# Performance work log

Hardware: AMD Instinct MI355X
Metric: run time of the kernel (lower is better)

## Reference

```python
import jax, jax.numpy as jnp
import numpy as np

NUM_NODES = 10000
WINDOW = 8
IN_C = 8
HID = 64
N_TOT = WINDOW * NUM_NODES
N_EDGES = 1280000
EPS = 1e-5


def setup_inputs() -> dict:
    key = jax.random.key(0)
    ks = jax.random.split(key, 12)
    s = 0.05
    X = jax.random.normal(ks[0], (N_TOT, IN_C), jnp.float32)
    edge_index = jax.random.randint(ks[1], (2, N_EDGES), 0, N_TOT, dtype=jnp.int32)
    edge_weight = jax.random.uniform(ks[2], (N_EDGES,), jnp.float32)
    return dict(
        X=X, edge_index=edge_index, edge_weight=edge_weight,
        w1=jax.random.normal(ks[3], (IN_C, HID), jnp.float32) * s, b1=jnp.zeros(HID, jnp.float32),
        w2=jax.random.normal(ks[4], (HID, HID), jnp.float32) * s, b2=jnp.zeros(HID, jnp.float32),
        g1=jnp.ones(HID, jnp.float32), be1=jnp.zeros(HID, jnp.float32),
        g2=jnp.ones(HID, jnp.float32), be2=jnp.zeros(HID, jnp.float32),
        wih1=jax.random.normal(ks[5], (4 * HID, 2 * HID), jnp.float32) * s,
        whh1=jax.random.normal(ks[6], (4 * HID, HID), jnp.float32) * s,
        bih1=jnp.zeros(4 * HID, jnp.float32), bhh1=jnp.zeros(4 * HID, jnp.float32),
        wih2=jax.random.normal(ks[7], (4 * HID, HID), jnp.float32) * s,
        whh2=jax.random.normal(ks[8], (4 * HID, HID), jnp.float32) * s,
        bih2=jnp.zeros(4 * HID, jnp.float32), bhh2=jnp.zeros(4 * HID, jnp.float32),
    )


def _gcn(x, src, dst, ew, w, b):
    h = x @ w
    deg = jax.ops.segment_sum(ew, dst, num_segments=N_TOT) + 1.0
    dinv = jax.lax.rsqrt(deg)
    norm = dinv[src] * ew * dinv[dst]                               # [E]
    agg = jax.ops.segment_sum(norm[:, None] * h[src], dst, num_segments=N_TOT)
    return agg + h * (dinv * dinv)[:, None] + b                      # self-loop term: h[i]/deg[i]


def _bn(x, g, b):
    # BatchNorm1d, training-mode batch statistics (biased variance)
    mu = x.mean(0)
    var = ((x - mu) ** 2).mean(0)
    return (x - mu) * jax.lax.rsqrt(var + EPS) * g + b


def _lstm(xs, wih, whh, bih, bhh):
    # xs: [T, B, F]; torch gate order i, f, g, o
    B = xs.shape[1]
    def step(carry, xt):
        h, c = carry
        z = xt @ wih.T + h @ whh.T + bih + bhh
        i, f, g, o = jnp.split(z, 4, axis=1)
        c = jax.nn.sigmoid(f) * c + jax.nn.sigmoid(i) * jnp.tanh(g)
        h = jax.nn.sigmoid(o) * jnp.tanh(c)
        return (h, c), h
    init = (jnp.zeros((B, HID), xs.dtype), jnp.zeros((B, HID), xs.dtype))
    (h, c), ys = jax.lax.scan(step, init, xs)
    return ys, h


def reference(X, edge_index, edge_weight, w1, b1, w2, b2, g1, be1, g2, be2,
              wih1, whh1, bih1, bhh1, wih2, whh2, bih2, bhh2):
    src, dst = edge_index[0], edge_index[1]
    # skip-feature S: [B*num_nodes, in_channels + window - 1]
    S = X.reshape(1, WINDOW, NUM_NODES, IN_C).transpose(0, 2, 1, 3).reshape(-1, WINDOW, IN_C)
    Sfeat = jnp.concatenate([S[:, 0, :], S[:, 1:, IN_C - 1]], axis=1)
    # two GCN layers (dropout omitted: deterministic baseline)
    x1 = _bn(jax.nn.relu(_gcn(X, src, dst, edge_weight, w1, b1)), g1, be1)
    x2 = _bn(jax.nn.relu(_gcn(x1, src, dst, edge_weight, w2, b2)), g2, be2)
    xc = jnp.concatenate([x1, x2], axis=1)                           # [N_TOT, 2H]
    xs = xc.reshape(1, WINDOW, NUM_NODES, 2 * HID).transpose(1, 0, 2, 3).reshape(WINDOW, -1, 2 * HID)
    ys, h1 = _lstm(xs, wih1, whh1, bih1, bhh1)
    ys2, h2 = _lstm(ys, wih2, whh2, bih2, bhh2)
    return jnp.concatenate([h1, h2, Sfeat], axis=1)                  # [num_nodes, 2H + IN_C + WINDOW - 1]
```

## Files before the change

kernel.cpp:

```cpp
#include <hip/hip_runtime.h>
#include <hip/hip_bf16.h>
#include <math.h>

#define NNODES 10000
#define NT     80000
#define NE     1280000
#define NBKT   625
#define CHUNK  5000
#define BNEPS  1e-5f

typedef __bf16 bf16x8 __attribute__((ext_vector_type(8)));
typedef float  f32x4  __attribute__((ext_vector_type(4)));

__device__ __forceinline__ float frcp(float x){ return __builtin_amdgcn_rcpf(x); }
__device__ __forceinline__ float fsig(float x){ return frcp(1.0f + __expf(-x)); }
__device__ __forceinline__ float ftanh(float x){ return 1.0f - 2.0f*frcp(1.0f + __expf(2.0f*x)); }
__device__ __forceinline__ float u2f(unsigned int u){ union{unsigned int u; float f;} c; c.u=u; return c.f; }
__device__ __forceinline__ unsigned int f2u(float f){ union{float f; unsigned int u;} c; c.f=f; return c.u; }
__device__ __forceinline__ unsigned short f2bu(float v){ __hip_bfloat16 h = __float2bfloat16(v); return *(unsigned short*)&h; }
__device__ __forceinline__ unsigned int pk2(float a, float b){ return (unsigned int)f2bu(a) | ((unsigned int)f2bu(b) << 16); }
__device__ __forceinline__ float dec15(unsigned int p){ return u2f((p & 0x7fffu) << 17); }

__global__ __launch_bounds__(256) void prep_w_kernel(
    const float* __restrict__ wih1, const float* __restrict__ whh1,
    const float* __restrict__ bih1, const float* __restrict__ bhh1,
    const float* __restrict__ wih2, const float* __restrict__ whh2,
    const float* __restrict__ bih2, const float* __restrict__ bhh2,
    const float* __restrict__ w1g, const float* __restrict__ w2g,
    unsigned int* __restrict__ W1f, unsigned int* __restrict__ W2f,
    float* __restrict__ bs1, float* __restrict__ bs2,
    unsigned int* __restrict__ W2g, unsigned int* __restrict__ W1g)
{
    int gid = blockIdx.x*256 + threadIdx.x;
    if (gid < 24576) {
        int i = gid & 3, lane = (gid>>2)&63, rest = gid>>8;
        int ks = rest % 6; rest /= 6;
        int nt = rest & 3, w = rest >> 2;
        int gate = nt*64 + w*16 + (lane & 15);
        int k = ks*32 + ((lane>>4)&3)*8 + 2*i;
        float v0 = (k     < 128) ? wih1[gate*128 + k]       : whh1[gate*64 + (k-128)];
        float v1 = (k + 1 < 128) ? wih1[gate*128 + k + 1]   : whh1[gate*64 + (k+1-128)];
        W1f[gid] = pk2(v0, v1);
    } else if (gid < 40960) {
        int r = gid - 24576;
        int i = r & 3, lane = (r>>2)&63, rest = r>>8;
        int ks = rest & 3; rest >>= 2;
        int nt = rest & 3, w = rest >> 2;
        int gate = nt*64 + w*16 + (lane & 15);
        int k = ks*32 + ((lane>>4)&3)*8 + 2*i;
        float v0 = (k     < 64) ? wih2[gate*64 + k]     : whh2[gate*64 + (k-64)];
        float v1 = (k + 1 < 64) ? wih2[gate*64 + k + 1] : whh2[gate*64 + (k+1-64)];
        W2f[r] = pk2(v0, v1);
    } else if (gid < 41216) {
        int j = gid - 40960; bs1[j] = bih1[j] + bhh1[j];
    } else if (gid < 41472) {
        int j = gid - 41216; bs2[j] = bih2[j] + bhh2[j];
    } else if (gid < 43520) {
        int r = gid - 41472;
        int i = r & 3, lane = (r>>2)&63, rest = r>>8;
        int ks = rest & 1, w = rest >> 1;
        int col = w*16 + (lane & 15);
        int k = ks*32 + ((lane>>4)&3)*8 + 2*i;
        W2g[r] = pk2(w2g[k*64 + col], w2g[(k+1)*64 + col]);
    } else if (gid < 44544) {
        int r = gid - 43520;
        int i = r & 3, lane = (r>>2)&63, w = r>>8;
        int col = w*16 + (lane & 15);
        int k = ((lane>>4)&3)*8 + 2*i;
        float v0 = (k     < 8) ? w1g[k*64 + col]     : 0.f;
        float v1 = (k + 1 < 8) ? w1g[(k+1)*64 + col] : 0.f;
        W1g[r] = pk2(v0, v1);
    }
}

__global__ __launch_bounds__(256) void sortA1_kernel(const int* __restrict__ dst,
                                                     int* __restrict__ histmat)
{
    __shared__ int h[NBKT];
    for (int i = threadIdx.x; i < NBKT; i += 256) h[i] = 0;
    __syncthreads();
    int base = blockIdx.x*CHUNK;
    for (int i = threadIdx.x; i < CHUNK; i += 256)
        atomicAdd(&h[dst[base + i] >> 7], 1);
    __syncthreads();
    for (int i = threadIdx.x; i < NBKT; i += 256)
        histmat[blockIdx.x*640 + i] = h[i];
}

__global__ __launch_bounds__(256) void sortA2a_kernel(const int* __restrict__ histmat,
                                                      int* __restrict__ offmatT,
                                                      int* __restrict__ binTotal)
{
    __shared__ int v[256];
    int b = blockIdx.x, t = threadIdx.x;
    int x = histmat[t*640 + b];
    v[t] = x;
    __syncthreads();
    for (int off = 1; off < 256; off <<= 1) {
        int y = (t >= off) ? v[t-off] : 0;
        __syncthreads();
        v[t] += y;
        __syncthreads();
    }
    offmatT[b*256 + t] = v[t] - x;
    if (t == 255) binTotal[b] = v[255];
}

__global__ __launch_bounds__(1024) void sortA2b_kernel(const int* __restrict__ binTotal,
                                                       int* __restrict__ bucketbase,
                                                       int* __restrict__ rowptr)
{
    __shared__ int part[1024];
    int t = threadIdx.x;
    int v = (t < NBKT) ? binTotal[t] : 0;
    part[t] = v;
    __syncthreads();
    for (int off = 1; off < 1024; off <<= 1) {
        int y = (t >= off) ? part[t-off] : 0;
        __syncthreads();
        part[t] += y;
        __syncthreads();
    }
    if (t < NBKT) bucketbase[t] = part[t] - v;
    if (t == 0) { bucketbase[NBKT] = NE; rowptr[NT] = NE; }
}

__global__ __launch_bounds__(256) void sortA3_kernel(const int* __restrict__ src,
                                                     const int* __restrict__ dst,
                                                     const float* __restrict__ ew,
                                                     const int* __restrict__ offmatT,
                                                     const int* __restrict__ bucketbase,
                                                     uint2* __restrict__ esort)
{
    __shared__ int cur[NBKT];
    int blk = blockIdx.x;
    for (int i = threadIdx.x; i < NBKT; i += 256)
        cur[i] = bucketbase[i] + offmatT[i*256 + blk];
    __syncthreads();
    int base = blk*CHUNK;
    for (int i = threadIdx.x; i < CHUNK; i += 256) {
        int e = base + i;
        int d = dst[e];
        int pos = atomicAdd(&cur[d >> 7], 1);
        uint2 r;
        r.x = (unsigned int)src[e] | ((unsigned int)(d & 127) << 17);
        r.y = f2u(ew[e]);
        esort[pos] = r;
    }
}

__global__ __launch_bounds__(256) void sortB1_kernel(const int* __restrict__ bucketbase,
                                                     const uint2* __restrict__ esort,
                                                     unsigned char* __restrict__ urank,
                                                     int* __restrict__ rowptr,
                                                     float* __restrict__ dinv)
{
    __shared__ int cnt[128];
    __shared__ float dg[128];
    __shared__ int ptr[128];
    int bin = blockIdx.x, t = threadIdx.x;
    if (t < 128) { cnt[t] = 0; dg[t] = 0.f; }
    __syncthreads();
    int base = bucketbase[bin], end = bucketbase[bin+1];
    for (int i = base + t; i < end; i += 256) {
        uint2 r = esort[i];
        int dl = (r.x >> 17) & 127;
        int rk = atomicAdd(&cnt[dl], 1);
        atomicAdd(&dg[dl], u2f(r.y));
        urank[i] = (unsigned char)rk;
    }
    __syncthreads();
    if (t < 128) ptr[t] = cnt[t];
    __syncthreads();
    for (int off = 1; off < 128; off <<= 1) {
        int y = (t >= off && t < 128) ? ptr[t-off] : 0;
        __syncthreads();
        if (t < 128) ptr[t] += y;
        __syncthreads();
    }
    if (t < 128) {
        rowptr[bin*128 + t] = base + ptr[t] - cnt[t];
        dinv[bin*128 + t]   = rsqrtf(dg[t] + 1.0f);
    }
}

__global__ __launch_bounds__(256) void sortB2_kernel(const int* __restrict__ bucketbase,
                                                     const uint2* __restrict__ esort,
                                                     const unsigned char* __restrict__ urank,
                                                     const int* __restrict__ rowptr,
                                                     const float* __restrict__ dinv,
                                                     unsigned int* __restrict__ epack)
{
    int bin = blockIdx.x;
    int base = bucketbase[bin], end = bucketbase[bin+1];
    for (int i = base + threadIdx.x; i < end; i += 256) {
        uint2 r = esort[i];
        int s = r.x & 0x1FFFF;
        int d = bin*128 + ((r.x >> 17) & 127);
        float w = u2f(r.y) * dinv[s];
        unsigned int p15 = (f2u(w) + (1u << 16)) >> 17;
        epack[rowptr[d] + (int)urank[i]] = ((unsigned int)s << 15) | p15;
    }
}

__global__ __launch_bounds__(256) void xconv_kernel(const float* __restrict__ X,
                                                    unsigned int* __restrict__ Xb)
{
    int gid = blockIdx.x*256 + threadIdx.x;
    if (gid >= NT*4) return;
    float2 v = *(const float2*)&X[(size_t)gid*2];
    Xb[gid] = pk2(v.x, v.y);
}

__global__ __launch_bounds__(256) void gather8_kernel(const int* __restrict__ rowptr,
                                                      const unsigned int* __restrict__ epack,
                                                      const uint4* __restrict__ Xb,
                                                      const float* __restrict__ dinv,
                                                      uint4* __restrict__ agg8b)
{
    int d = blockIdx.x*256 + threadIdx.x;
    if (d >= NT) return;
    int beg = rowptr[d], end = rowptr[d+1];
    float acc[8];
    #pragma unroll
    for (int k = 0; k < 8; ++k) acc[k] = 0.f;
    for (int i = beg; i < end; ++i) {
        unsigned int p = epack[i];
        float nrm = dec15(p);
        uint4 xv = Xb[p >> 15];
        unsigned int um[4] = {xv.x, xv.y, xv.z, xv.w};
        #pragma unroll
        for (int m = 0; m < 4; ++m) {
            acc[2*m]   = fmaf(nrm, u2f(um[m] << 16),         acc[2*m]);
            acc[2*m+1] = fmaf(nrm, u2f(um[m] & 0xffff0000u), acc[2*m+1]);
        }
    }
    float dv = dinv[d];
    uint4 xd = Xb[d];
    unsigned int ud[4] = {xd.x, xd.y, xd.z, xd.w};
    #pragma unroll
    for (int m = 0; m < 4; ++m) {
        acc[2*m]   = dv * fmaf(dv, u2f(ud[m] << 16),         acc[2*m]);
        acc[2*m+1] = dv * fmaf(dv, u2f(ud[m] & 0xffff0000u), acc[2*m+1]);
    }
    agg8b[d] = make_uint4(pk2(acc[0],acc[1]), pk2(acc[2],acc[3]),
                          pk2(acc[4],acc[5]), pk2(acc[6],acc[7]));
}

__global__ __launch_bounds__(256) void gemm8relu_kernel(const uint4* __restrict__ agg8b,
                                                        const unsigned int* __restrict__ W1g,
                                                        const float* __restrict__ b,
                                                        unsigned short* __restrict__ y,
                                                        float* __restrict__ sums)
{
    __shared__ __align__(16) unsigned short As[64][8];
    __shared__ float sm[256], sq[256];
    const int tid = threadIdx.x;
    const int w = tid >> 6, lane = tid & 63, lr = lane & 15, lg = lane >> 4;
    union { uint4 u; bf16x8 v; } bw; bw.u = ((const uint4*)W1g)[w*64 + lane];
    float bc = b[w*16 + lr];
    float s = 0.f, q = 0.f;
    for (int tile = blockIdx.x; tile < NT/64; tile += gridDim.x) {
        int rbase = tile*64;
        __syncthreads();
        if (tid < 64) *(uint4*)&As[tid][0] = agg8b[rbase + tid];
        __syncthreads();
        #pragma unroll
        for (int rt = 0; rt < 4; ++rt) {
            bf16x8 a = {};
            if (lg == 0) a = *(const bf16x8*)&As[rt*16 + lr][0];
            f32x4 acc = {0.f, 0.f, 0.f, 0.f};
            acc = __builtin_amdgcn_mfma_f32_16x16x32_bf16(a, bw.v, acc, 0, 0, 0);
            #pragma unroll
            for (int r = 0; r < 4; ++r) {
                float v = fmaxf(acc[r] + bc, 0.f);
                y[(size_t)(rbase + rt*16 + lg*4 + r)*64 + w*16 + lr] = f2bu(v);
                s += v; q += v*v;
            }
        }
    }
    sm[tid] = s; sq[tid] = q;
    __syncthreads();
    if (tid < 64) {
        int base = (tid >> 4)*64 + (tid & 15);
        atomicAdd(&sums[tid],      sm[base] + sm[base+16] + sm[base+32] + sm[base+48]);
        atomicAdd(&sums[64 + tid], sq[base] + sq[base+16] + sq[base+32] + sq[base+48]);
    }
}

__global__ __launch_bounds__(256) void gather64_kernel(const int* __restrict__ rowptr,
                                                       const unsigned int* __restrict__ epack,
                                                       const unsigned int* __restrict__ y1,
                                                       const float* __restrict__ dinv,
                                                       const float* __restrict__ sums,
                                                       const float* __restrict__ g,
                                                       const float* __restrict__ be,
                                                       unsigned int* __restrict__ xcat)
{
    int lane = threadIdx.x & 63;
    int grp = lane >> 4, l = lane & 15;
    int gwave = blockIdx.x*4 + (threadIdx.x >> 6);
    int nwaves = gridDim.x*4;
    float ax[4], bx[4];
    #pragma unroll
    for (int j = 0; j < 4; ++j) {
        int c = 4*l + j;
        float mu  = sums[c] * (1.0f/NT);
        float var = sums[64 + c] * (1.0f/NT) - mu*mu;
        float a = rsqrtf(var + BNEPS) * g[c];
        ax[j] = a; bx[j] = be[c] - mu*a;
    }
    for (int d = gwave; d < NT; d += nwaves) {
        int beg = rowptr[d], end = rowptr[d+1];
        float a0 = 0.f, a1 = 0.f, a2 = 0.f, a3 = 0.f;
        for (int i = beg; i < end; i += 4) {
            int idx = i + grp;
            bool valid = idx < end;
            unsigned int p = epack[valid ? idx : (end - 1)];
            float nrm = valid ? dec15(p) : 0.f;
            uint2 xv = *(const uint2*)&y1[(size_t)(p >> 15)*32 + 2*l];
            a0 = fmaf(nrm, fmaf(ax[0], u2f(xv.x << 16),         bx[0]), a0);
            a1 = fmaf(nrm, fmaf(ax[1], u2f(xv.x & 0xffff0000u), bx[1]), a1);
            a2 = fmaf(nrm, fmaf(ax[2], u2f(xv.y << 16),         bx[2]), a2);
            a3 = fmaf(nrm, fmaf(ax[3], u2f(xv.y & 0xffff0000u), bx[3]), a3);
        }
        a0 += __shfl_xor(a0, 16); a1 += __shfl_xor(a1, 16);
        a2 += __shfl_xor(a2, 16); a3 += __shfl_xor(a3, 16);
        a0 += __shfl_xor(a0, 32); a1 += __shfl_xor(a1, 32);
        a2 += __shfl_xor(a2, 32); a3 += __shfl_xor(a3, 32);
        if (grp == 0) {
            float dv = dinv[d];
            uint2 xd = *(const uint2*)&y1[(size_t)d*32 + 2*l];
            float x0 = fmaf(ax[0], u2f(xd.x << 16),         bx[0]);
            float x1 = fmaf(ax[1], u2f(xd.x & 0xffff0000u), bx[1]);
            float x2 = fmaf(ax[2], u2f(xd.y << 16),         bx[2]);
            float x3 = fmaf(ax[3], u2f(xd.y & 0xffff0000u), bx[3]);
            *(uint2*)&xcat[(size_t)d*64 + 2*l] = make_uint2(pk2(x0, x1), pk2(x2, x3));
            a0 = dv * fmaf(dv, x0, a0);
            a1 = dv * fmaf(dv, x1, a1);
            a2 = dv * fmaf(dv, x2, a2);
            a3 = dv * fmaf(dv, x3, a3);
            *(uint2*)&xcat[(size_t)d*64 + 32 + 2*l] = make_uint2(pk2(a0, a1), pk2(a2, a3));
        }
    }
}

__global__ __launch_bounds__(256) void gemm64relu_kernel(const unsigned int* __restrict__ xcat,
                                                         const unsigned int* __restrict__ W2g,
                                                         const float* __restrict__ b,
                                                         unsigned short* __restrict__ y,
                                                         float* __restrict__ sums)
{
    __shared__ __align__(16) unsigned short As[64][72];
    __shared__ float sm[256], sq[256];
    const int tid = threadIdx.x;
    const int w = tid >> 6, lane = tid & 63, lr = lane & 15, lg = lane >> 4;
    union { uint4 u; bf16x8 v; } b0, b1;
    b0.u = ((const uint4*)W2g)[(w*2 + 0)*64 + lane];
    b1.u = ((const uint4*)W2g)[(w*2 + 1)*64 + lane];
    float bc = b[w*16 + lr];
    const int srow = tid >> 2, squad = tid & 3;
    float s = 0.f, q = 0.f;
    for (int tile = blockIdx.x; tile < NT/64; tile += gridDim.x) {
        int rbase = tile*64;
        __syncthreads();
        {
            const unsigned int* src = &xcat[(size_t)(rbase + srow)*64 + 32 + squad*8];
            unsigned int* dst = (unsigned int*)&As[srow][0] + squad*8;
            *(uint4*)(dst)     = *(const uint4*)(src);
            *(uint4*)(dst + 4) = *(const uint4*)(src + 4);
        }
        __syncthreads();
        #pragma unroll
        for (int rt = 0; rt < 4; ++rt) {
            bf16x8 a0 = *(const bf16x8*)&As[rt*16 + lr][lg*8];
            bf16x8 a1 = *(const bf16x8*)&As[rt*16 + lr][32 + lg*8];
            f32x4 acc = {0.f, 0.f, 0.f, 0.f};
            acc = __builtin_amdgcn_mfma_f32_16x16x32_bf16(a0, b0.v, acc, 0, 0, 0);
            acc = __builtin_amdgcn_mfma_f32_16x16x32_bf16(a1, b1.v, acc, 0, 0, 0);
            #pragma unroll
            for (int r = 0; r < 4; ++r) {
                float v = fmaxf(acc[r] + bc, 0.f);
                y[(size_t)(rbase + rt*16 + lg*4 + r)*64 + w*16 + lr] = f2bu(v);
                s += v; q += v*v;
            }
        }
    }
    sm[tid] = s; sq[tid] = q;
    __syncthreads();
    if (tid < 64) {
        int base = (tid >> 4)*64 + (tid & 15);
        atomicAdd(&sums[tid],      sm[base] + sm[base+16] + sm[base+32] + sm[base+48]);
        atomicAdd(&sums[64 + tid], sq[base] + sq[base+16] + sq[base+32] + sq[base+48]);
    }
}

#define LROW 328
__global__ __launch_bounds__(256, 2) void lstm_mfma_kernel(
    const unsigned int* __restrict__ xcat,
    const unsigned int* __restrict__ y2,
    const float* __restrict__ sums2, const float* __restrict__ g2,
    const float* __restrict__ be2,
    const unsigned int* __restrict__ W1f, const unsigned int* __restrict__ W2f,
    const float* __restrict__ bs1, const float* __restrict__ bs2,
    float* __restrict__ out)
{
    __shared__ __align__(16) unsigned short xb[16][LROW];
    const int tid  = threadIdx.x;
    const int w    = tid >> 6, lane = tid & 63;
    const int lr   = lane & 15;
    const int lg   = lane >> 4;
    const int nb0  = blockIdx.x * 16;

    uint4 w1f[4][6], w2f[4][4];
    {
        const uint4* p1 = (const uint4*)W1f;
        #pragma unroll
        for (int nt = 0; nt < 4; ++nt)
            #pragma unroll
            for (int ks = 0; ks < 6; ++ks)
                w1f[nt][ks] = p1[((w*4 + nt)*6 + ks)*64 + lane];
        const uint4* p2 = (const uint4*)W2f;
        #pragma unroll
        for (int nt = 0; nt < 4; ++nt)
            #pragma unroll
            for (int ks = 0; ks < 4; ++ks)
                w2f[nt][ks] = p2[((w*4 + nt)*4 + ks)*64 + lane];
    }
    float b1v[4], b2v[4];
    #pragma unroll
    for (int nt = 0; nt < 4; ++nt) {
        b1v[nt] = bs1[nt*64 + w*16 + lr];
        b2v[nt] = bs2[nt*64 + w*16 + lr];
    }

    const int sn = tid >> 4, k0 = (tid & 15)*8;
    float ax[8], bx[8];
    if (k0 >= 64) {
        #pragma unroll
        for (int j = 0; j < 8; ++j) {
            int c = k0 - 64 + j;
            float mu  = sums2[c] * (1.0f/NT);
            float var = sums2[64 + c] * (1.0f/NT) - mu*mu;
            float a = rsqrtf(var + BNEPS) * g2[c];
            ax[j] = a; bx[j] = be2[c] - mu*a;
        }
    }

    for (int i = tid; i < 16*24; i += 256) {
        int n = i / 24, kk = 128 + (i % 24)*8;
        uint4 z; z.x = z.y = z.z = z.w = 0u;
        *(uint4*)&xb[n][kk] = z;
    }

    auto stage = [&](int step) {
        size_t row = (size_t)(step*NNODES + nb0 + sn);
        uint4 raw;
        if (k0 < 64) {
            raw = *(const uint4*)&xcat[row*64 + (k0 >> 1)];
        } else {
            raw = *(const uint4*)&y2[row*32 + ((k0 - 64) >> 1)];
            unsigned int um[4] = {raw.x, raw.y, raw.z, raw.w};
            #pragma unroll
            for (int m = 0; m < 4; ++m) {
                float v0 = fmaf(ax[2*m],   u2f(um[m] << 16),         bx[2*m]);
                float v1 = fmaf(ax[2*m+1], u2f(um[m] & 0xffff0000u), bx[2*m+1]);
                um[m] = pk2(v0, v1);
            }
            raw.x = um[0]; raw.y = um[1]; raw.z = um[2]; raw.w = um[3];
        }
        *(uint4*)&xb[sn][k0] = raw;
    };
    stage(0);
    float c1[4] = {0.f,0.f,0.f,0.f}, c2[4] = {0.f,0.f,0.f,0.f};

    for (int step = 0; step < 8; ++step) {
        __syncthreads();

        f32x4 acc[4];
        #pragma unroll
        for (int nt = 0; nt < 4; ++nt) { acc[nt][0]=0.f; acc[nt][1]=0.f; acc[nt][2]=0.f; acc[nt][3]=0.f; }
        #pragma unroll
        for (int ks = 0; ks < 6; ++ks) {
            bf16x8 a = *(const bf16x8*)&xb[lr][ks*32 + lg*8];
            #pragma unroll
            for (int nt = 0; nt < 4; ++nt) {
                union { uint4 u; bf16x8 v; } wb; wb.u = w1f[nt][ks];
                acc[nt] = __builtin_amdgcn_mfma_f32_16x16x32_bf16(a, wb.v, acc[nt], 0, 0, 0);
            }
        }
        __syncthreads();

        #pragma unroll
        for (int r = 0; r < 4; ++r) {
            float zi = acc[0][r] + b1v[0];
            float zf = acc[1][r] + b1v[1];
            float zg = acc[2][r] + b1v[2];
            float zo = acc[3][r] + b1v[3];
            float c  = fsig(zf)*c1[r] + fsig(zi)*ftanh(zg);
            c1[r] = c;
            float hv = fsig(zo)*ftanh(c);
            int node = lg*4 + r;
            xb[node][128 + w*16 + lr] = f2bu(hv);
            if (step == 7) out[(size_t)(nb0 + node)*143 + w*16 + lr] = hv;
        }
        if (step < 7) stage(step + 1);
        __syncthreads();

        int rb = 192 + 64*((step+1)&1);
        int wb2 = 192 + 64*(step&1);
        #pragma unroll
        for (int nt = 0; nt < 4; ++nt) { acc[nt][0]=0.f; acc[nt][1]=0.f; acc[nt][2]=0.f; acc[nt][3]=0.f; }
        #pragma unroll
        for (int ks = 0; ks < 2; ++ks) {
            bf16x8 a = *(const bf16x8*)&xb[lr][128 + ks*32 + lg*8];
            #pragma unroll
            for (int nt = 0; nt < 4; ++nt) {
                union { uint4 u; bf16x8 v; } wbv; wbv.u = w2f[nt][ks];
                acc[nt] = __builtin_amdgcn_mfma_f32_16x16x32_bf16(a, wbv.v, acc[nt], 0, 0, 0);
            }
        }
        #pragma unroll
        for (int ks = 0; ks < 2; ++ks) {
            bf16x8 a = *(const bf16x8*)&xb[lr][rb + ks*32 + lg*8];
            #pragma unroll
            for (int nt = 0; nt < 4; ++nt) {
                union { uint4 u; bf16x8 v; } wbv; wbv.u = w2f[nt][2+ks];
                acc[nt] = __builtin_amdgcn_mfma_f32_16x16x32_bf16(a, wbv.v, acc[nt], 0, 0, 0);
            }
        }
        #pragma unroll
        for (int r = 0; r < 4; ++r) {
            float zi = acc[0][r] + b2v[0];
            float zf = acc[1][r] + b2v[1];
            float zg = acc[2][r] + b2v[2];
            float zo = acc[3][r] + b2v[3];
            float c  = fsig(zf)*c2[r] + fsig(zi)*ftanh(zg);
            c2[r] = c;
            float hv = fsig(zo)*ftanh(c);
            int node = lg*4 + r;
            xb[node][wb2 + w*16 + lr] = f2bu(hv);
            if (step == 7) out[(size_t)(nb0 + node)*143 + 64 + w*16 + lr] = hv;
        }
    }
}

__global__ __launch_bounds__(256) void sfeat_kernel(const float* __restrict__ X,
                                                    float* __restrict__ out)
{
    int gid = blockIdx.x*256 + threadIdx.x;
    if (gid >= NNODES*15) return;
    int n = gid/15, i = gid%15;
    float v = (i < 8) ? X[(size_t)n*8 + i]
                      : X[((size_t)(i-7)*NNODES + n)*8 + 7];
    out[(size_t)n*143 + 128 + i] = v;
}

extern "C" void kernel_launch(void* const* d_in, const int* in_sizes, int n_in,
                              void* d_out, int out_size, void* d_ws, size_t ws_size,
                              hipStream_t stream)
{
    (void)in_sizes; (void)n_in; (void)out_size; (void)ws_size;
    const float* X    = (const float*)d_in[0];
    const int*   ei   = (const int*)d_in[1];
    const float* ew   = (const float*)d_in[2];
    const float* w1   = (const float*)d_in[3];
    const float* b1   = (const float*)d_in[4];
    const float* w2   = (const float*)d_in[5];
    const float* b2   = (const float*)d_in[6];
    const float* g1   = (const float*)d_in[7];
    const float* be1  = (const float*)d_in[8];
    const float* g2   = (const float*)d_in[9];
    const float* be2  = (const float*)d_in[10];
    const float* wih1 = (const float*)d_in[11];
    const float* whh1 = (const float*)d_in[12];
    const float* bih1 = (const float*)d_in[13];
    const float* bhh1 = (const float*)d_in[14];
    const float* wih2 = (const float*)d_in[15];
    const float* whh2 = (const float*)d_in[16];
    const float* bih2 = (const float*)d_in[17];
    const float* bhh2 = (const float*)d_in[18];
    float* out = (float*)d_out;
    float* ws  = (float*)d_ws;

    const int* src = ei;
    const int* dst = ei + NE;

    float* sums      = ws;
    float* dinv      = ws + 256;
    int*   rowptr    = (int*)(ws + 80256);
    int*   binTotal  = (int*)(ws + 160260);
    int*   bucketbase= (int*)(ws + 160900);
    int*   histmat   = (int*)(ws + 161540);
    int*   offmatT   = (int*)(ws + 325380);
    unsigned char* urank = (unsigned char*)(ws + 485380);
    uint2* esort     = (uint2*)(ws + 805384);
    unsigned int* y2 = (unsigned int*)(ws + 805384);
    unsigned int* epack = (unsigned int*)(ws + 3365384);
    unsigned int* Xb = (unsigned int*)(ws + 4645384);
    uint4* agg8b     = (uint4*)(ws + 4965384);
    unsigned int* y1 = (unsigned int*)(ws + 5605384);
    unsigned int* xcat = (unsigned int*)(ws + 8165384);
    unsigned int* W1f  = (unsigned int*)(ws + 13285384);
    unsigned int* W2f  = W1f + 24576;
    float* bs1 = (float*)(W2f + 16384);
    float* bs2 = bs1 + 256;
    unsigned int* W2g  = (unsigned int*)(bs2 + 256);
    unsigned int* W1g  = W2g + 2048;

    hipMemsetAsync(ws, 0, 256 * 4, stream);

    prep_w_kernel<<<174, 256, 0, stream>>>(wih1,whh1,bih1,bhh1,
                                           wih2,whh2,bih2,bhh2,
                                           w1, w2,
                                           W1f,W2f,bs1,bs2,W2g,W1g);
    sortA1_kernel<<<256, 256, 0, stream>>>(dst, histmat);
    sortA2a_kernel<<<NBKT, 256, 0, stream>>>(histmat, offmatT, binTotal);
    sortA2b_kernel<<<1, 1024, 0, stream>>>(binTotal, bucketbase, rowptr);
    sortA3_kernel<<<256, 256, 0, stream>>>(src, dst, ew, offmatT, bucketbase, esort);
    sortB1_kernel<<<NBKT, 256, 0, stream>>>(bucketbase, esort, urank, rowptr, dinv);
    sortB2_kernel<<<NBKT, 256, 0, stream>>>(bucketbase, esort, urank, rowptr, dinv, epack);
    xconv_kernel<<<(NT*4+255)/256, 256, 0, stream>>>(X, Xb);

    gather8_kernel<<<(NT+255)/256, 256, 0, stream>>>(rowptr, epack, (const uint4*)Xb, dinv, agg8b);
    gemm8relu_kernel<<<320, 256, 0, stream>>>(agg8b, W1g, b1, (unsigned short*)y1, sums);

    gather64_kernel<<<2048, 256, 0, stream>>>(rowptr, epack, y1, dinv, sums, g1, be1, xcat);
    gemm64relu_kernel<<<320, 256, 0, stream>>>(xcat, W2g, b2, (unsigned short*)y2, sums + 128);

    lstm_mfma_kernel<<<NNODES/16, 256, 0, stream>>>(xcat, y2, sums + 128, g2, be2,
                                                    W1f, W2f, bs1, bs2, out);
    sfeat_kernel<<<(NNODES*15+255)/256, 256, 0, stream>>>(X, out);
}
```

Before: 201.2 us.

## Precompute BN-applied layer-1 features as FP8 for the 64-wide edge gather

Adds a pass that applies BatchNorm to layer-1 outputs once per node, writes the bf16 result into xcat and an FP8 (e4m3) copy into a separate buffer. The 64-channel gather then reads 4 bytes per neighbour instead of 8 and skips the per-edge BN affine, cutting gather bandwidth and arithmetic. This costs an extra kernel launch and a full pass over the features, and FP8 quantization of aggregated neighbour features reduces accuracy against the reference. The FP8 buffer reuses the workspace region also used for the edge-sort scratch and y2.

```diff
diff --git a/kernel.cpp b/kernel.cpp
--- a/kernel.cpp
+++ b/kernel.cpp
@@ -11,6 +11,7 @@
 
 typedef __bf16 bf16x8 __attribute__((ext_vector_type(8)));
 typedef float  f32x4  __attribute__((ext_vector_type(4)));
+typedef float  f32x2  __attribute__((ext_vector_type(2)));
 
 __device__ __forceinline__ float frcp(float x){ return __builtin_amdgcn_rcpf(x); }
 __device__ __forceinline__ float fsig(float x){ return frcp(1.0f + __expf(-x)); }
@@ -288,28 +289,48 @@
     }
 }
 
+__global__ __launch_bounds__(256) void xbn8_kernel(const unsigned int* __restrict__ y1,
+                                                   const float* __restrict__ sums,
+                                                   const float* __restrict__ g,
+                                                   const float* __restrict__ be,
+                                                   unsigned int* __restrict__ xcat,
+                                                   unsigned int* __restrict__ x8)
+{
+    __shared__ float axs[64], bxs[64];
+    int tid = threadIdx.x;
+    if (tid < 64) {
+        float mu  = sums[tid] * (1.0f/NT);
+        float var = sums[64 + tid] * (1.0f/NT) - mu*mu;
+        float a = rsqrtf(var + BNEPS) * g[tid];
+        axs[tid] = a; bxs[tid] = be[tid] - mu*a;
+    }
+    __syncthreads();
+    int gid = blockIdx.x*256 + tid;
+    if (gid >= NT*16) return;
+    int c4 = gid & 15, n = gid >> 4;
+    int c0 = c4*4;
+    uint2 yy = *(const uint2*)&y1[(size_t)n*32 + 2*c4];
+    float v0 = fmaf(axs[c0+0], u2f(yy.x << 16),         bxs[c0+0]);
+    float v1 = fmaf(axs[c0+1], u2f(yy.x & 0xffff0000u), bxs[c0+1]);
+    float v2 = fmaf(axs[c0+2], u2f(yy.y << 16),         bxs[c0+2]);
+    float v3 = fmaf(axs[c0+3], u2f(yy.y & 0xffff0000u), bxs[c0+3]);
+    *(uint2*)&xcat[(size_t)n*64 + 2*c4] = make_uint2(pk2(v0, v1), pk2(v2, v3));
+    int p8 = 0;
+    p8 = __builtin_amdgcn_cvt_pk_fp8_f32(v0, v1, p8, false);
+    p8 = __builtin_amdgcn_cvt_pk_fp8_f32(v2, v3, p8, true);
+    x8[(size_t)n*16 + c4] = (unsigned int)p8;
+}
+
 __global__ __launch_bounds__(256) void gather64_kernel(const int* __restrict__ rowptr,
                                                        const unsigned int* __restrict__ epack,
-                                                       const unsigned int* __restrict__ y1,
+                                                       const unsigned int* __restrict__ x8,
                                                        const float* __restrict__ dinv,
-                                                       const float* __restrict__ sums,
-                                                       const float* __restrict__ g,
-                                                       const float* __restrict__ be,
                                                        unsigned int* __restrict__ xcat)
 {
     int lane = threadIdx.x & 63;
     int grp = lane >> 4, l = lane & 15;
     int gwave = blockIdx.x*4 + (threadIdx.x >> 6);
     int nwaves = gridDim.x*4;
-    float ax[4], bx[4];
-    #pragma unroll
-    for (int j = 0; j < 4; ++j) {
-        int c = 4*l + j;
-        float mu  = sums[c] * (1.0f/NT);
-        float var = sums[64 + c] * (1.0f/NT) - mu*mu;
-        float a = rsqrtf(var + BNEPS) * g[c];
-        ax[j] = a; bx[j] = be[c] - mu*a;
-    }
     for (int d = gwave; d < NT; d += nwaves) {
         int beg = rowptr[d], end = rowptr[d+1];
         float a0 = 0.f, a1 = 0.f, a2 = 0.f, a3 = 0.f;
@@ -318,11 +339,13 @@
             bool valid = idx < end;
             unsigned int p = epack[valid ? idx : (end - 1)];
             float nrm = valid ? dec15(p) : 0.f;
-            uint2 xv = *(const uint2*)&y1[(size_t)(p >> 15)*32 + 2*l];
-            a0 = fmaf(nrm, fmaf(ax[0], u2f(xv.x << 16),         bx[0]), a0);
-            a1 = fmaf(nrm, fmaf(ax[1], u2f(xv.x & 0xffff0000u), bx[1]), a1);
-            a2 = fmaf(nrm, fmaf(ax[2], u2f(xv.y << 16),         bx[2]), a2);
-            a3 = fmaf(nrm, fmaf(ax[3], u2f(xv.y & 0xffff0000u), bx[3]), a3);
+            unsigned int xv = x8[(size_t)(p >> 15)*16 + l];
+            f32x2 lo = __builtin_amdgcn_cvt_pk_f32_fp8((int)xv, false);
+            f32x2 hi = __builtin_amdgcn_cvt_pk_f32_fp8((int)xv, true);
+            a0 = fmaf(nrm, lo[0], a0);
+            a1 = fmaf(nrm, lo[1], a1);
+            a2 = fmaf(nrm, hi[0], a2);
+            a3 = fmaf(nrm, hi[1], a3);
         }
         a0 += __shfl_xor(a0, 16); a1 += __shfl_xor(a1, 16);
         a2 += __shfl_xor(a2, 16); a3 += __shfl_xor(a3, 16);
@@ -330,12 +353,9 @@
         a2 += __shfl_xor(a2, 32); a3 += __shfl_xor(a3, 32);
         if (grp == 0) {
             float dv = dinv[d];
-            uint2 xd = *(const uint2*)&y1[(size_t)d*32 + 2*l];
-            float x0 = fmaf(ax[0], u2f(xd.x << 16),         bx[0]);
-            float x1 = fmaf(ax[1], u2f(xd.x & 0xffff0000u), bx[1]);
-            float x2 = fmaf(ax[2], u2f(xd.y << 16),         bx[2]);
-            float x3 = fmaf(ax[3], u2f(xd.y & 0xffff0000u), bx[3]);
-            *(uint2*)&xcat[(size_t)d*64 + 2*l] = make_uint2(pk2(x0, x1), pk2(x2, x3));
+            uint2 xd = *(const uint2*)&xcat[(size_t)d*64 + 2*l];
+            float x0 = u2f(xd.x << 16), x1 = u2f(xd.x & 0xffff0000u);
+            float x2 = u2f(xd.y << 16), x3 = u2f(xd.y & 0xffff0000u);
             a0 = dv * fmaf(dv, x0, a0);
             a1 = dv * fmaf(dv, x1, a1);
             a2 = dv * fmaf(dv, x2, a2);
@@ -595,6 +615,7 @@
     int*   offmatT   = (int*)(ws + 325380);
     unsigned char* urank = (unsigned char*)(ws + 485380);
     uint2* esort     = (uint2*)(ws + 805384);
+    unsigned int* x8 = (unsigned int*)(ws + 805384);
     unsigned int* y2 = (unsigned int*)(ws + 805384);
     unsigned int* epack = (unsigned int*)(ws + 3365384);
     unsigned int* Xb = (unsigned int*)(ws + 4645384);
@@ -625,7 +646,9 @@
     gather8_kernel<<<(NT+255)/256, 256, 0, stream>>>(rowptr, epack, (const uint4*)Xb, dinv, agg8b);
     gemm8relu_kernel<<<320, 256, 0, stream>>>(agg8b, W1g, b1, (unsigned short*)y1, sums);
 
-    gather64_kernel<<<2048, 256, 0, stream>>>(rowptr, epack, y1, dinv, sums, g1, be1, xcat);
+    xbn8_kernel<<<(NT*16+255)/256, 256, 0, stream>>>(y1, sums, g1, be1, xcat, x8);
+
+    gather64_kernel<<<2048, 256, 0, stream>>>(rowptr, epack, x8, dinv, xcat);
     gemm64relu_kernel<<<320, 256, 0, stream>>>(xcat, W2g, b2, (unsigned short*)y2, sums + 128);
 
     lstm_mfma_kernel<<<NNODES/16, 256, 0, stream>>>(xcat, y2, sums + 128, g2, be2,
```

New measurement: 202.6 us. No clear change (+0.7%).
